# Performance work log

Measured on AMD Instinct MI355X. Metric: run time of the kernel, lower is better.

The kernel has to match this reference:

```python
import jax, jax.numpy as jnp
import numpy as np

B, S, D = 2, 2048, 2048
H = 16
NOPE, ROPE, VH = 128, 64, 128
QR, KVR = 512, 512
EPS = 1e-6


def _rmsnorm(x, w):
    return x * jax.lax.rsqrt(jnp.mean(x * x, axis=-1, keepdims=True) + EPS) * w


def _rope(t, freqs_cis):
    # t: (B, h, S, ROPE); freqs_cis: (S, ROPE//2, 2) as (cos, sin)
    b, h, s, d = t.shape
    t2 = t.reshape(b, h, s, d // 2, 2)
    cos = freqs_cis[:, :, 0][None, None]  # (1,1,S,ROPE//2)
    sin = freqs_cis[:, :, 1][None, None]
    x0, x1 = t2[..., 0], t2[..., 1]
    r0 = x0 * cos - x1 * sin
    r1 = x0 * sin + x1 * cos
    return jnp.stack([r0, r1], axis=-1).reshape(b, h, s, d)


def setup_inputs() -> dict:
    key = jax.random.key(0)
    ks = jax.random.split(key, 11)
    def init(k, out_dim, in_dim):
        return jax.random.normal(k, (out_dim, in_dim), jnp.float32) * (1.0 / np.sqrt(in_dim))
    x = jax.random.normal(ks[0], (B, S, D), jnp.float32)
    half = ROPE // 2
    inv = 1.0 / (10000.0 ** (np.arange(half, dtype=np.float64) / half))
    ang = np.outer(np.arange(S), inv)
    freqs_cis = jnp.asarray(np.stack([np.cos(ang), np.sin(ang)], axis=-1), jnp.float32)  # (S, half, 2)
    mask = jnp.ones((S, S), dtype=bool)  # unused (is_causal=True in original)
    return {
        "x": x,
        "mask": mask,
        "freqs_cis": freqs_cis,
        "w_cq": init(ks[1], QR, D),
        "w_qnorm": jnp.ones((QR,), jnp.float32),
        "w_dqn": init(ks[2], H * NOPE, QR),
        "w_dqr": init(ks[3], H * ROPE, QR),
        "w_ckv": init(ks[4], KVR, D),
        "w_kvnorm": jnp.ones((KVR,), jnp.float32),
        "w_dkn": init(ks[5], H * NOPE, KVR),
        "w_dv": init(ks[6], H * VH, KVR),
        "w_krope": init(ks[7], ROPE, D),
        "w_proj": init(ks[8], D, H * VH),
    }


def reference(x, mask, freqs_cis, w_cq, w_qnorm, w_dqn, w_dqr, w_ckv, w_kvnorm, w_dkn, w_dv, w_krope, w_proj):
    b, s, _ = x.shape
    # Q path: compress -> RMSNorm -> decompress (nope, rope)
    cq = jnp.einsum('bsd,rd->bsr', x, w_cq)
    nq = _rmsnorm(cq, w_qnorm)
    q_nope = jnp.einsum('bsr,er->bse', nq, w_dqn).reshape(b, s, H, NOPE).transpose(0, 2, 1, 3)
    q_rope = jnp.einsum('bsr,er->bse', nq, w_dqr).reshape(b, s, H, ROPE).transpose(0, 2, 1, 3)
    # KV path
    ckv = jnp.einsum('bsd,rd->bsr', x, w_ckv)
    nkv = _rmsnorm(ckv, w_kvnorm)
    k_nope = jnp.einsum('bsr,er->bse', nkv, w_dkn).reshape(b, s, H, NOPE).transpose(0, 2, 1, 3)
    value = jnp.einsum('bsr,er->bse', nkv, w_dv).reshape(b, s, H, VH).transpose(0, 2, 1, 3)
    # shared single-head rope key, scaled by 1/num_heads
    k_rope = jnp.einsum('bsd,ed->bse', x, w_krope).reshape(b, s, 1, ROPE).transpose(0, 2, 1, 3) / H
    # partial RoPE
    q_rope = _rope(q_rope, freqs_cis)
    k_rope = _rope(k_rope, freqs_cis)
    # recombine nope|rope
    q = jnp.concatenate([q_nope, q_rope], axis=-1)  # (B,H,S,NOPE+ROPE)
    k = jnp.concatenate([k_nope, jnp.broadcast_to(k_rope, (b, H, s, ROPE))], axis=-1)
    # causal SDPA
    scale = 1.0 / np.sqrt(NOPE + ROPE)
    scores = jnp.einsum('bhqd,bhkd->bhqk', q, k) * scale
    causal = jnp.tril(jnp.ones((s, s), dtype=bool))
    scores = jnp.where(causal[None, None], scores, -jnp.inf)
    attn = jax.nn.softmax(scores, axis=-1)
    out = jnp.einsum('bhqk,bhkv->bhqv', attn, value)  # (B,H,S,VH)
    out = out.transpose(0, 2, 1, 3).reshape(b, s, H * VH)
    return jnp.einsum('bse,de->bsd', out, w_proj)
```

## Files before the change

kernel.cpp:

```cpp
#include <hip/hip_runtime.h>
#include <hip/hip_bf16.h>


typedef __attribute__((ext_vector_type(8))) short s8v;
typedef __attribute__((ext_vector_type(4))) float f4v;

#define DEV static __device__ __forceinline__

DEV ushort f2b(float f) {
  __hip_bfloat16 h = __float2bfloat16(f);
  return *reinterpret_cast<ushort*>(&h);
}
DEV float b2f(ushort u) {
  __hip_bfloat16 h = *reinterpret_cast<__hip_bfloat16*>(&u);
  return __bfloat162float(h);
}
DEV f4v mfma16(s8v a, s8v b, f4v c) {
  return __builtin_amdgcn_mfma_f32_16x16x32_bf16(a, b, c, 0, 0, 0);
}
DEV void gload16(const ushort* g, ushort* l) {
  __builtin_amdgcn_global_load_lds((const __attribute__((address_space(1))) void*)g,
                                   (__attribute__((address_space(3))) void*)l, 16, 0, 0);
}
DEV void barrier_raw() {
  __builtin_amdgcn_sched_barrier(0);
  __builtin_amdgcn_s_barrier();
  __builtin_amdgcn_sched_barrier(0);
}

struct CastSeg { const float* src; ushort* dst; int n4; int blk0; };
struct CastTab { CastSeg seg[10]; };

__global__ __launch_bounds__(256) void cast_all_kernel(CastTab t) {
  int b = blockIdx.x;
  int si = 0;
#pragma unroll
  for (int i = 1; i < 10; ++i) si = (b >= t.seg[i].blk0) ? i : si;
  int i4 = (b - t.seg[si].blk0) * 256 + threadIdx.x;
  if (i4 >= t.seg[si].n4) return;
  ushort4 o;
  if (t.seg[si].src) {
    float4 v = reinterpret_cast<const float4*>(t.seg[si].src)[i4];
    o.x = f2b(v.x); o.y = f2b(v.y); o.z = f2b(v.z); o.w = f2b(v.w);
  } else {
    o = ushort4{0, 0, 0, 0};
  }
  reinterpret_cast<ushort4*>(t.seg[si].dst)[i4] = o;
}

template <bool BF16OUT>
DEV void gemm_core(const ushort* __restrict__ A, const ushort* __restrict__ B,
                   void* __restrict__ C, int N, int K, int row0, int col0,
                   ushort* a_lds0, ushort* a_lds1, ushort* b_lds0, ushort* b_lds1) {
  const int tid = threadIdx.x;
  const int lane = tid & 63, wv = tid >> 6;
  const int wm = wv >> 1, wn = wv & 1;
  const int l15 = lane & 15, l4 = lane >> 4;
  const int srow = lane >> 2;
  const int scol = (lane & 3) * 8;
  ushort* a_lds[2] = {a_lds0, a_lds1};
  ushort* b_lds[2] = {b_lds0, b_lds1};

  f4v acc[4][4];
#pragma unroll
  for (int i = 0; i < 4; ++i)
#pragma unroll
    for (int j = 0; j < 4; ++j) acc[i][j] = f4v{0.f, 0.f, 0.f, 0.f};

  auto stage = [&](int k0, int bsel) {
#pragma unroll
    for (int i = 0; i < 2; ++i) {
      int s = wv * 2 + i;
      gload16(&A[(size_t)(row0 + s * 16 + srow) * K + k0 + scol], &a_lds[bsel][s * 512]);
      gload16(&B[(size_t)(col0 + s * 16 + srow) * K + k0 + scol], &b_lds[bsel][s * 512]);
    }
  };

  stage(0, 0);
  int cur = 0;
  for (int k0 = 0; k0 < K; k0 += 32) {
    __syncthreads();
    if (k0 + 32 < K) stage(k0 + 32, cur ^ 1);
    s8v af[4], bfr[4];
#pragma unroll
    for (int mi = 0; mi < 4; ++mi)
      af[mi] = *reinterpret_cast<const s8v*>(&a_lds[cur][(wm * 64 + mi * 16 + l15) * 32 + 8 * l4]);
#pragma unroll
    for (int ni = 0; ni < 4; ++ni)
      bfr[ni] = *reinterpret_cast<const s8v*>(&b_lds[cur][(wn * 64 + ni * 16 + l15) * 32 + 8 * l4]);
#pragma unroll
    for (int mi = 0; mi < 4; ++mi)
#pragma unroll
      for (int ni = 0; ni < 4; ++ni) acc[mi][ni] = mfma16(af[mi], bfr[ni], acc[mi][ni]);
    cur ^= 1;
  }

#pragma unroll
  for (int mi = 0; mi < 4; ++mi)
#pragma unroll
    for (int ni = 0; ni < 4; ++ni)
#pragma unroll
      for (int j = 0; j < 4; ++j) {
        int r = row0 + wm * 64 + mi * 16 + l4 * 4 + j;
        int cl = col0 + wn * 64 + ni * 16 + l15;
        if (BF16OUT)
          reinterpret_cast<ushort*>(C)[(size_t)r * N + cl] = f2b(acc[mi][ni][j]);
        else
          reinterpret_cast<float*>(C)[(size_t)r * N + cl] = acc[mi][ni][j];
      }
}

template <bool BF16OUT>
__global__ __launch_bounds__(256) void gemm_bt(const ushort* __restrict__ A,
                                               const ushort* __restrict__ B,
                                               void* __restrict__ C, int N, int K) {
  __shared__ ushort a0[128 * 32], a1[128 * 32], b0[128 * 32], b1[128 * 32];
  gemm_core<BF16OUT>(A, B, C, N, K, blockIdx.x * 128, blockIdx.y * 128, a0, a1, b0, b1);
}

__global__ __launch_bounds__(256) void gemm2_dual(const ushort* __restrict__ nq,
                                                  const ushort* __restrict__ w2q,
                                                  ushort* __restrict__ g2q,
                                                  const ushort* __restrict__ nkv,
                                                  const ushort* __restrict__ w2kv,
                                                  ushort* __restrict__ g2kv) {
  __shared__ ushort a0[128 * 32], a1[128 * 32], b0[128 * 32], b1[128 * 32];
  int by = blockIdx.y;
  if (by < 24)
    gemm_core<true>(nq, w2q, g2q, 3072, 512, blockIdx.x * 128, by * 128, a0, a1, b0, b1);
  else
    gemm_core<true>(nkv, w2kv, g2kv, 4096, 512, blockIdx.x * 128, (by - 24) * 128, a0, a1, b0, b1);
}

__global__ __launch_bounds__(256) void norm_rope1_kernel(
    const float* __restrict__ g1, const float* __restrict__ wq, const float* __restrict__ wkv,
    const float* __restrict__ freqs, ushort* __restrict__ nq, ushort* __restrict__ nkv,
    ushort* __restrict__ kro) {
  const int m = blockIdx.x;
  const int s = m & 2047;
  const int tid = threadIdx.x;
  __shared__ float red[4];
  const float* row = g1 + (size_t)m * 1152;

  float v0 = row[tid], v1 = row[tid + 256];
  float ss = v0 * v0 + v1 * v1;
#pragma unroll
  for (int off = 32; off > 0; off >>= 1) ss += __shfl_down(ss, off);
  if ((tid & 63) == 0) red[tid >> 6] = ss;
  __syncthreads();
  float r = rsqrtf((red[0] + red[1] + red[2] + red[3]) * (1.0f / 512.0f) + 1e-6f);
  nq[(size_t)m * 512 + tid] = f2b(v0 * r * wq[tid]);
  nq[(size_t)m * 512 + tid + 256] = f2b(v1 * r * wq[tid + 256]);

  float u0 = row[512 + tid], u1 = row[512 + tid + 256];
  float ss2 = u0 * u0 + u1 * u1;
#pragma unroll
  for (int off = 32; off > 0; off >>= 1) ss2 += __shfl_down(ss2, off);
  __syncthreads();
  if ((tid & 63) == 0) red[tid >> 6] = ss2;
  __syncthreads();
  float r2 = rsqrtf((red[0] + red[1] + red[2] + red[3]) * (1.0f / 512.0f) + 1e-6f);
  nkv[(size_t)m * 512 + tid] = f2b(u0 * r2 * wkv[tid]);
  nkv[(size_t)m * 512 + tid + 256] = f2b(u1 * r2 * wkv[tid + 256]);

  if (tid < 32) {
    float x0 = row[1024 + 2 * tid], x1 = row[1024 + 2 * tid + 1];
    float c = freqs[s * 64 + 2 * tid], sn = freqs[s * 64 + 2 * tid + 1];
    kro[(size_t)m * 64 + 2 * tid] = f2b((x0 * c - x1 * sn) * (1.0f / 16.0f));
    kro[(size_t)m * 64 + 2 * tid + 1] = f2b((x0 * sn + x1 * c) * (1.0f / 16.0f));
  }
}

__global__ __launch_bounds__(256) void misc_fused_kernel(ushort* __restrict__ g2q,
                                                         const float* __restrict__ freqs,
                                                         const ushort* __restrict__ g2kv,
                                                         ushort* __restrict__ vT) {
  const int tid = threadIdx.x;
  if (blockIdx.x < 2048) {
    int blk = blockIdx.x;
    int bh = blk >> 6;
    int rem = blk & 63;
    int st = rem >> 1, dt = rem & 1;
    int b = bh >> 4, h = bh & 15;
    __shared__ ushort t[64][72];
#pragma unroll
    for (int it = 0; it < 2; ++it) {
      int c = tid + it * 256;
      int sl = c >> 3, cc = (c & 7) * 8;
      *reinterpret_cast<uint4*>(&t[sl][cc]) = *reinterpret_cast<const uint4*>(
          &g2kv[(size_t)(b * 2048 + st * 64 + sl) * 4096 + 2048 + h * 128 + dt * 64 + cc]);
    }
    __syncthreads();
#pragma unroll
    for (int it = 0; it < 2; ++it) {
      int c = tid + it * 256;
      int dl = c >> 3, cc = (c & 7) * 8;
      ushort tmp[8];
#pragma unroll
      for (int e = 0; e < 8; ++e) tmp[e] = t[cc + e][dl];
      *reinterpret_cast<uint4*>(&vT[(size_t)(bh * 128 + dt * 64 + dl) * 2048 + st * 64 + cc]) =
          *reinterpret_cast<uint4*>(tmp);
    }
  } else {
    int idx = (blockIdx.x - 2048) * 256 + tid;
    int m = idx >> 9;
    int rem = idx & 511;
    int h = rem >> 5, j = rem & 31;
    int s = m & 2047;
    size_t base = (size_t)m * 3072 + 2048 + h * 64 + 2 * j;
    ushort2 pr = *reinterpret_cast<ushort2*>(&g2q[base]);
    float x0 = b2f(pr.x), x1 = b2f(pr.y);
    float c = freqs[s * 64 + 2 * j], sn = freqs[s * 64 + 2 * j + 1];
    ushort2 o;
    o.x = f2b(x0 * c - x1 * sn);
    o.y = f2b(x0 * sn + x1 * c);
    *reinterpret_cast<ushort2*>(&g2q[base]) = o;
  }
}

__global__ __launch_bounds__(512, 4) void attn_kernel(const ushort* __restrict__ q,
                                                      const ushort* __restrict__ knope,
                                                      const ushort* __restrict__ kro,
                                                      const ushort* __restrict__ vT,
                                                      ushort* __restrict__ out) {
  const int p = blockIdx.x;
  const int bh = 4 * (p & 7) + ((p >> 3) & 3);
  const int qt = 15 - (p >> 5);
  const int b = bh >> 4, h = bh & 15;
  const int tid = threadIdx.x, lane = tid & 63, w = tid >> 6;
  const int l15 = lane & 15, l4 = lane >> 4;

  __shared__ ushort kbuf[2][64 * 192];
  __shared__ ushort vbuf[128 * 64];
  __shared__ ushort p_lds[8][1024];

  s8v qf[6];
  {
    const size_t qbase = (size_t)(b * 2048 + qt * 128 + w * 16 + l15) * 3072;
#pragma unroll
    for (int kc = 0; kc < 4; ++kc)
      qf[kc] = *reinterpret_cast<const s8v*>(&q[qbase + h * 128 + kc * 32 + 8 * l4]);
#pragma unroll
    for (int kc = 4; kc < 6; ++kc)
      qf[kc] = *reinterpret_cast<const s8v*>(&q[qbase + 2048 + h * 64 + (kc - 4) * 32 + 8 * l4]);
  }

  f4v oacc[8];
#pragma unroll
  for (int i = 0; i < 8; ++i) oacc[i] = f4v{0.f, 0.f, 0.f, 0.f};
  float m_r[4] = {-INFINITY, -INFINITY, -INFINITY, -INFINITY};
  float l_r[4] = {0.f, 0.f, 0.f, 0.f};
  const float sc2 = 0.07216878364870323f * 1.44269504f;
  const int nkt = 2 * qt + 2;
  const int kbase = b * 2048;

  auto stageK = [&](int kt, int bsel) {
    const int krow0 = kbase + kt * 64;
#pragma unroll
    for (int i = 0; i < 3; ++i) {
      int s = w * 3 + i;
      int pp = s * 1024 + lane * 16;
      int row = pp / 384;
      int col = ((pp ^ ((row & 7) << 4)) - row * 384) >> 1;
      const ushort* src = (col < 128)
          ? &knope[(size_t)(krow0 + row) * 4096 + h * 128 + col]
          : &kro[(size_t)(krow0 + row) * 64 + (col - 128)];
      gload16(src, &kbuf[bsel][s * 512]);
    }
  };
  auto stageV = [&](int kt) {
#pragma unroll
    for (int i = 0; i < 2; ++i) {
      int s = w * 2 + i;
      int pp = s * 1024 + lane * 16;
      int d = pp >> 7;
      int key = ((pp ^ ((d & 7) << 4)) & 127) >> 1;
      gload16(&vT[(size_t)(bh * 128 + d) * 2048 + kt * 64 + key], &vbuf[s * 512]);
    }
  };

  stageK(0, 0);
  int cur = 0;
  for (int kt = 0; kt < nkt; ++kt) {
    asm volatile("s_waitcnt vmcnt(0)" ::: "memory");
    barrier_raw();
    stageV(kt);
    if (kt + 1 < nkt) stageK(kt + 1, cur ^ 1);
    const char* kb = (const char*)kbuf[cur];

    f4v sacc[4];
    __builtin_amdgcn_s_setprio(1);
#pragma unroll
    for (int nb = 0; nb < 4; ++nb) {
      sacc[nb] = f4v{0.f, 0.f, 0.f, 0.f};
      const int row = nb * 16 + l15;
      const int sw = (row & 7) << 4;
#pragma unroll
      for (int kc = 0; kc < 6; ++kc) {
        s8v bfr = *reinterpret_cast<const s8v*>(kb + row * 384 + ((kc * 64 + l4 * 16) ^ sw));
        sacc[nb] = mfma16(qf[kc], bfr, sacc[nb]);
      }
    }
    __builtin_amdgcn_s_setprio(0);

    const int qrow0 = qt * 128 + w * 16 + l4 * 4;
#pragma unroll
    for (int nb = 0; nb < 4; ++nb) {
      int key = kt * 64 + nb * 16 + l15;
#pragma unroll
      for (int j = 0; j < 4; ++j) {
        float sv = sacc[nb][j] * sc2;
        if (kt >= 2 * qt && key > qrow0 + j) sv = -INFINITY;
        sacc[nb][j] = sv;
      }
    }
    float mx[4];
#pragma unroll
    for (int j = 0; j < 4; ++j)
      mx[j] = fmaxf(fmaxf(sacc[0][j], sacc[1][j]), fmaxf(sacc[2][j], sacc[3][j]));
#pragma unroll
    for (int off = 1; off < 16; off <<= 1)
#pragma unroll
      for (int j = 0; j < 4; ++j) mx[j] = fmaxf(mx[j], __shfl_xor(mx[j], off));

    float need = fmaxf(fmaxf(mx[0] - m_r[0], mx[1] - m_r[1]),
                       fmaxf(mx[2] - m_r[2], mx[3] - m_r[3]));
    if (!__all(need <= 8.0f)) {
      float al[4];
#pragma unroll
      for (int j = 0; j < 4; ++j) {
        float mnew = fmaxf(m_r[j], mx[j]);
        al[j] = exp2f(m_r[j] - mnew);
        m_r[j] = mnew;
        l_r[j] *= al[j];
      }
#pragma unroll
      for (int nv = 0; nv < 8; ++nv)
#pragma unroll
        for (int j = 0; j < 4; ++j) oacc[nv][j] *= al[j];
    }
    float rs[4] = {0.f, 0.f, 0.f, 0.f};
#pragma unroll
    for (int nb = 0; nb < 4; ++nb)
#pragma unroll
      for (int j = 0; j < 4; ++j) {
        float pv = exp2f(sacc[nb][j] - m_r[j]);
        sacc[nb][j] = pv;
        rs[j] += pv;
      }
#pragma unroll
    for (int off = 1; off < 16; off <<= 1)
#pragma unroll
      for (int j = 0; j < 4; ++j) rs[j] += __shfl_xor(rs[j], off);
#pragma unroll
    for (int j = 0; j < 4; ++j) l_r[j] += rs[j];
#pragma unroll
    for (int nb = 0; nb < 4; ++nb)
#pragma unroll
      for (int j = 0; j < 4; ++j) {
        int r = l4 * 4 + j;
        p_lds[w][r * 64 + ((nb * 16 + l15) ^ ((r & 7) << 3))] = f2b(sacc[nb][j]);
      }

    if (kt + 1 < nkt) {
      asm volatile("s_waitcnt vmcnt(3)" ::: "memory");
    } else {
      asm volatile("s_waitcnt vmcnt(0)" ::: "memory");
    }
    barrier_raw();

    const char* vb = (const char*)vbuf;
    __builtin_amdgcn_s_setprio(1);
#pragma unroll
    for (int kc2 = 0; kc2 < 2; ++kc2) {
      s8v pf = *reinterpret_cast<const s8v*>(
          &p_lds[w][l15 * 64 + ((kc2 * 32 + 8 * l4) ^ ((l15 & 7) << 3))]);
#pragma unroll
      for (int nv = 0; nv < 8; ++nv) {
        const int d = nv * 16 + l15;
        s8v vf = *reinterpret_cast<const s8v*>(vb + d * 128 + ((kc2 * 64 + l4 * 16) ^ ((d & 7) << 4)));
        oacc[nv] = mfma16(pf, vf, oacc[nv]);
      }
    }
    __builtin_amdgcn_s_setprio(0);
    cur ^= 1;
  }

#pragma unroll
  for (int j = 0; j < 4; ++j) {
    float inv = 1.0f / l_r[j];
    int m = b * 2048 + qt * 128 + w * 16 + l4 * 4 + j;
#pragma unroll
    for (int nv = 0; nv < 8; ++nv)
      out[(size_t)m * 2048 + h * 128 + nv * 16 + l15] = f2b(oacc[nv][j] * inv);
  }
}

extern "C" void kernel_launch(void* const* d_in, const int* in_sizes, int n_in,
                              void* d_out, int out_size, void* d_ws, size_t ws_size,
                              hipStream_t stream) {
  const float* x       = (const float*)d_in[0];
  const float* freqs   = (const float*)d_in[2];
  const float* w_cq    = (const float*)d_in[3];
  const float* w_qnorm = (const float*)d_in[4];
  const float* w_dqn   = (const float*)d_in[5];
  const float* w_dqr   = (const float*)d_in[6];
  const float* w_ckv   = (const float*)d_in[7];
  const float* w_kvnorm= (const float*)d_in[8];
  const float* w_dkn   = (const float*)d_in[9];
  const float* w_dv    = (const float*)d_in[10];
  const float* w_krope = (const float*)d_in[11];
  const float* w_proj  = (const float*)d_in[12];
  float* out = (float*)d_out;

  char* ws = (char*)d_ws;
  const size_t MB = 1ull << 20;
  ushort* g2kv = (ushort*)(ws + 0);
  float*  g1   = (float*) (ws + 0);
  ushort* g2q  = (ushort*)(ws + 32 * MB);
  ushort* xbf  = (ushort*)(ws + 32 * MB);
  ushort* w1   = (ushort*)(ws + 48 * MB);
  ushort* vT   = (ushort*)(ws + 56 * MB);
  ushort* nq   = (ushort*)(ws + 56 * MB);
  ushort* nkv  = (ushort*)(ws + 60 * MB);
  ushort* w2q  = (ushort*)(ws + 64 * MB);
  ushort* w2kv = (ushort*)(ws + 67 * MB);
  ushort* att  = (ushort*)(ws + 72 * MB);
  ushort* wpj  = (ushort*)(ws + 88 * MB);
  ushort* kro  = (ushort*)(ws + 96 * MB);

  CastTab t;
  const float* srcs[10] = {x, w_cq, w_ckv, w_krope, nullptr,
                           w_dqn, w_dqr, w_dkn, w_dv, w_proj};
  ushort* dsts[10] = {xbf, w1, w1 + 512 * 2048, w1 + 1024 * 2048, w1 + 1088 * 2048,
                      w2q, w2q + 2048 * 512, w2kv, w2kv + 2048 * 512, wpj};
  int ns[10] = {4096 * 2048, 512 * 2048, 512 * 2048, 64 * 2048, 64 * 2048,
                2048 * 512, 1024 * 512, 2048 * 512, 2048 * 512, 2048 * 2048};
  int blk = 0;
  for (int i = 0; i < 10; ++i) {
    t.seg[i].src = srcs[i];
    t.seg[i].dst = dsts[i];
    t.seg[i].n4 = ns[i] / 4;
    t.seg[i].blk0 = blk;
    blk += (ns[i] / 4 + 255) / 256;
  }
  cast_all_kernel<<<blk, 256, 0, stream>>>(t);

  gemm_bt<false><<<dim3(32, 9), 256, 0, stream>>>(xbf, w1, g1, 1152, 2048);
  norm_rope1_kernel<<<4096, 256, 0, stream>>>(g1, w_qnorm, w_kvnorm, freqs, nq, nkv, kro);
  gemm2_dual<<<dim3(32, 56), 256, 0, stream>>>(nq, w2q, g2q, nkv, w2kv, g2kv);
  misc_fused_kernel<<<2048 + 8192, 256, 0, stream>>>(g2q, freqs, g2kv, vT);
  attn_kernel<<<512, 512, 0, stream>>>(g2q, g2kv, kro, vT, att);
  gemm_bt<false><<<dim3(32, 16), 256, 0, stream>>>(att, wpj, out, 2048, 2048);
}
```

Baseline: 489.5 us.

## Compute transposed S tile, keep P in registers via shuffles, reorder block schedule

After: 461.8 us. -5.7%, faster.

```diff
diff --git a/kernel.cpp b/kernel.cpp
--- a/kernel.cpp
+++ b/kernel.cpp
@@ -224,15 +224,15 @@
                                                       const ushort* __restrict__ vT,
                                                       ushort* __restrict__ out) {
   const int p = blockIdx.x;
-  const int bh = 4 * (p & 7) + ((p >> 3) & 3);
-  const int qt = 15 - (p >> 5);
+  const int a = (p >> 5) & 7;
+  const int qt = (p < 256) ? (15 - a) : a;
+  const int bh = p & 31;
   const int b = bh >> 4, h = bh & 15;
   const int tid = threadIdx.x, lane = tid & 63, w = tid >> 6;
   const int l15 = lane & 15, l4 = lane >> 4;
 
   __shared__ ushort kbuf[2][64 * 192];
   __shared__ ushort vbuf[128 * 64];
-  __shared__ ushort p_lds[8][1024];
 
   s8v qf[6];
   {
@@ -248,11 +248,11 @@
   f4v oacc[8];
 #pragma unroll
   for (int i = 0; i < 8; ++i) oacc[i] = f4v{0.f, 0.f, 0.f, 0.f};
-  float m_r[4] = {-INFINITY, -INFINITY, -INFINITY, -INFINITY};
-  float l_r[4] = {0.f, 0.f, 0.f, 0.f};
+  float m_r = -INFINITY, l_r = 0.f;
   const float sc2 = 0.07216878364870323f * 1.44269504f;
   const int nkt = 2 * qt + 2;
   const int kbase = b * 2048;
+  const int myq = qt * 128 + w * 16 + l15;
 
   auto stageK = [&](int kt, int bsel) {
     const int krow0 = kbase + kt * 64;
@@ -297,70 +297,75 @@
       const int sw = (row & 7) << 4;
 #pragma unroll
       for (int kc = 0; kc < 6; ++kc) {
-        s8v bfr = *reinterpret_cast<const s8v*>(kb + row * 384 + ((kc * 64 + l4 * 16) ^ sw));
-        sacc[nb] = mfma16(qf[kc], bfr, sacc[nb]);
+        s8v kf = *reinterpret_cast<const s8v*>(kb + row * 384 + ((kc * 64 + l4 * 16) ^ sw));
+        sacc[nb] = mfma16(kf, qf[kc], sacc[nb]);
       }
     }
     __builtin_amdgcn_s_setprio(0);
 
-    const int qrow0 = qt * 128 + w * 16 + l4 * 4;
 #pragma unroll
     for (int nb = 0; nb < 4; ++nb) {
-      int key = kt * 64 + nb * 16 + l15;
+      int key = kt * 64 + nb * 16 + 4 * l4;
 #pragma unroll
       for (int j = 0; j < 4; ++j) {
         float sv = sacc[nb][j] * sc2;
-        if (kt >= 2 * qt && key > qrow0 + j) sv = -INFINITY;
+        if (kt >= 2 * qt && key + j > myq) sv = -INFINITY;
         sacc[nb][j] = sv;
       }
     }
-    float mx[4];
-#pragma unroll
-    for (int j = 0; j < 4; ++j)
-      mx[j] = fmaxf(fmaxf(sacc[0][j], sacc[1][j]), fmaxf(sacc[2][j], sacc[3][j]));
-#pragma unroll
-    for (int off = 1; off < 16; off <<= 1)
-#pragma unroll
-      for (int j = 0; j < 4; ++j) mx[j] = fmaxf(mx[j], __shfl_xor(mx[j], off));
-
-    float need = fmaxf(fmaxf(mx[0] - m_r[0], mx[1] - m_r[1]),
-                       fmaxf(mx[2] - m_r[2], mx[3] - m_r[3]));
-    if (!__all(need <= 8.0f)) {
-      float al[4];
+    float mx = sacc[0][0];
+#pragma unroll
+    for (int nb = 0; nb < 4; ++nb)
+#pragma unroll
+      for (int j = 0; j < 4; ++j) mx = fmaxf(mx, sacc[nb][j]);
+    mx = fmaxf(mx, __shfl_xor(mx, 16));
+    mx = fmaxf(mx, __shfl_xor(mx, 32));
+
+    if (!__all(mx - m_r <= 8.0f)) {
+      float mnew = fmaxf(m_r, mx);
+      float al = exp2f(m_r - mnew);
+      m_r = mnew;
+      l_r *= al;
+      float alj[4];
+#pragma unroll
+      for (int j = 0; j < 4; ++j) alj[j] = __shfl(al, 4 * l4 + j);
+#pragma unroll
+      for (int nv = 0; nv < 8; ++nv)
+#pragma unroll
+        for (int j = 0; j < 4; ++j) oacc[nv][j] *= alj[j];
+    }
+    float rs = 0.f;
+#pragma unroll
+    for (int nb = 0; nb < 4; ++nb)
 #pragma unroll
       for (int j = 0; j < 4; ++j) {
-        float mnew = fmaxf(m_r[j], mx[j]);
-        al[j] = exp2f(m_r[j] - mnew);
-        m_r[j] = mnew;
-        l_r[j] *= al[j];
+        float pv = exp2f(sacc[nb][j] - m_r);
+        sacc[nb][j] = pv;
+        rs += pv;
       }
-#pragma unroll
-      for (int nv = 0; nv < 8; ++nv)
-#pragma unroll
-        for (int j = 0; j < 4; ++j) oacc[nv][j] *= al[j];
-    }
-    float rs[4] = {0.f, 0.f, 0.f, 0.f};
-#pragma unroll
-    for (int nb = 0; nb < 4; ++nb)
-#pragma unroll
-      for (int j = 0; j < 4; ++j) {
-        float pv = exp2f(sacc[nb][j] - m_r[j]);
-        sacc[nb][j] = pv;
-        rs[j] += pv;
-      }
-#pragma unroll
-    for (int off = 1; off < 16; off <<= 1)
-#pragma unroll
-      for (int j = 0; j < 4; ++j) rs[j] += __shfl_xor(rs[j], off);
-#pragma unroll
-    for (int j = 0; j < 4; ++j) l_r[j] += rs[j];
-#pragma unroll
-    for (int nb = 0; nb < 4; ++nb)
-#pragma unroll
-      for (int j = 0; j < 4; ++j) {
-        int r = l4 * 4 + j;
-        p_lds[w][r * 64 + ((nb * 16 + l15) ^ ((r & 7) << 3))] = f2b(sacc[nb][j]);
-      }
+    rs += __shfl_xor(rs, 16);
+    rs += __shfl_xor(rs, 32);
+    l_r += rs;
+
+    uint pkE[4], pkO[4];
+#pragma unroll
+    for (int nb = 0; nb < 4; ++nb) {
+      pkE[nb] = ((uint)f2b(sacc[nb][1]) << 16) | f2b(sacc[nb][0]);
+      pkO[nb] = ((uint)f2b(sacc[nb][3]) << 16) | f2b(sacc[nb][2]);
+    }
+    const int hi2 = l4 >> 1;
+    const int sbase = l15 + 16 * (2 * (l4 & 1));
+    union PF { uint u[4]; s8v v; } pf0, pf1;
+#pragma unroll
+    for (int t = 0; t < 4; ++t) {
+      int src = sbase + 16 * (t >> 1);
+      uint wa0 = __shfl((t & 1) ? pkO[0] : pkE[0], src);
+      uint wb0 = __shfl((t & 1) ? pkO[1] : pkE[1], src);
+      pf0.u[t] = hi2 ? wb0 : wa0;
+      uint wa1 = __shfl((t & 1) ? pkO[2] : pkE[2], src);
+      uint wb1 = __shfl((t & 1) ? pkO[3] : pkE[3], src);
+      pf1.u[t] = hi2 ? wb1 : wa1;
+    }
 
     if (kt + 1 < nkt) {
       asm volatile("s_waitcnt vmcnt(3)" ::: "memory");
@@ -373,26 +378,28 @@
     __builtin_amdgcn_s_setprio(1);
 #pragma unroll
     for (int kc2 = 0; kc2 < 2; ++kc2) {
-      s8v pf = *reinterpret_cast<const s8v*>(
-          &p_lds[w][l15 * 64 + ((kc2 * 32 + 8 * l4) ^ ((l15 & 7) << 3))]);
+      s8v pfr = kc2 ? pf1.v : pf0.v;
 #pragma unroll
       for (int nv = 0; nv < 8; ++nv) {
         const int d = nv * 16 + l15;
         s8v vf = *reinterpret_cast<const s8v*>(vb + d * 128 + ((kc2 * 64 + l4 * 16) ^ ((d & 7) << 4)));
-        oacc[nv] = mfma16(pf, vf, oacc[nv]);
+        oacc[nv] = mfma16(pfr, vf, oacc[nv]);
       }
     }
     __builtin_amdgcn_s_setprio(0);
     cur ^= 1;
   }
 
+  float invl = 1.0f / l_r;
+  float invj[4];
+#pragma unroll
+  for (int j = 0; j < 4; ++j) invj[j] = __shfl(invl, 4 * l4 + j);
 #pragma unroll
   for (int j = 0; j < 4; ++j) {
-    float inv = 1.0f / l_r[j];
-    int m = b * 2048 + qt * 128 + w * 16 + l4 * 4 + j;
+    int m = b * 2048 + qt * 128 + w * 16 + 4 * l4 + j;
 #pragma unroll
     for (int nv = 0; nv < 8; ++nv)
-      out[(size_t)m * 2048 + h * 128 + nv * 16 + l15] = f2b(oacc[nv][j] * inv);
+      out[(size_t)m * 2048 + h * 128 + nv * 16 + l15] = f2b(oacc[nv][j] * invj[j]);
   }
 }
 
```
